# Kernel tuning notes

Measured on AMD Instinct MI355X. Metric: run time of the kernel, lower is better.

## Reference

```python
import jax, jax.numpy as jnp
import numpy as np

EPS = 1e-7
POS_THR = 0.7
NEG_THR = 0.3


def _make_boxes(key, shape):
    # corner-format boxes (x1, y1, x2, y2) in [0, 1]
    k1, k2 = jax.random.split(key)
    center = jax.random.uniform(k1, shape[:-1] + (2,), minval=0.2, maxval=0.8)
    size = jax.random.uniform(k2, shape[:-1] + (2,), minval=0.05, maxval=0.3)
    return jnp.concatenate([center - size / 2, center + size / 2], axis=-1)


def setup_inputs() -> dict:
    key = jax.random.key(0)
    B, M, N, C = 16, 128, 25200, 80
    k1, k2, k3, k4, k5, k6 = jax.random.split(key, 6)
    label_box = _make_boxes(k1, (B, M, 4))
    # zero-pad ~half the label slots (padding convention detected via != 0)
    valid = jax.random.uniform(k2, (B, M)) < 0.5
    label_box = label_box * valid[:, :, None].astype(jnp.float32)
    label_cls = jax.random.randint(k3, (B, M), 0, C)
    # predictions: jittered copies of label boxes so positive matches exist
    assign = jnp.arange(N) % M  # [N]
    box = label_box[:, assign, :] + 0.01 * jax.random.normal(k4, (B, N, 4))
    prb = jax.random.uniform(k5, (B, N), minval=0.01, maxval=0.99)
    cls_logits = jax.random.normal(k6, (B, N, C))
    cls = jax.nn.softmax(cls_logits, axis=-1)
    return {
        'label_box': label_box,
        'box': box,
        'prb': prb,
        'cls': cls,
        'label_cls': label_cls,
    }


def _iou_matrix(a, b):
    # a: [B, M, 4], b: [B, N, 4] corner boxes -> [B, M, N]
    a = a[:, :, None, :]
    b = b[:, None, :, :]
    ix1 = jnp.maximum(a[..., 0], b[..., 0])
    iy1 = jnp.maximum(a[..., 1], b[..., 1])
    ix2 = jnp.minimum(a[..., 2], b[..., 2])
    iy2 = jnp.minimum(a[..., 3], b[..., 3])
    inter = jnp.clip(ix2 - ix1, 0) * jnp.clip(iy2 - iy1, 0)
    area_a = jnp.clip(a[..., 2] - a[..., 0], 0) * jnp.clip(a[..., 3] - a[..., 1], 0)
    area_b = jnp.clip(b[..., 2] - b[..., 0], 0) * jnp.clip(b[..., 3] - b[..., 1], 0)
    union = area_a + area_b - inter
    return inter / (union + EPS)


def _ciou_loss(b1, b2):
    # elementwise CIoU loss between matched corner boxes [..., 4]
    ix1 = jnp.maximum(b1[..., 0], b2[..., 0])
    iy1 = jnp.maximum(b1[..., 1], b2[..., 1])
    ix2 = jnp.minimum(b1[..., 2], b2[..., 2])
    iy2 = jnp.minimum(b1[..., 3], b2[..., 3])
    inter = jnp.clip(ix2 - ix1, 0) * jnp.clip(iy2 - iy1, 0)
    w1 = jnp.clip(b1[..., 2] - b1[..., 0], 0)
    h1 = jnp.clip(b1[..., 3] - b1[..., 1], 0)
    w2 = jnp.clip(b2[..., 2] - b2[..., 0], 0)
    h2 = jnp.clip(b2[..., 3] - b2[..., 1], 0)
    union = w1 * h1 + w2 * h2 - inter
    iou = inter / (union + EPS)
    # enclosing box diagonal
    cw = jnp.maximum(b1[..., 2], b2[..., 2]) - jnp.minimum(b1[..., 0], b2[..., 0])
    ch = jnp.maximum(b1[..., 3], b2[..., 3]) - jnp.minimum(b1[..., 1], b2[..., 1])
    c2 = cw * cw + ch * ch + EPS
    # center distance
    dx = (b1[..., 0] + b1[..., 2] - b2[..., 0] - b2[..., 2]) / 2
    dy = (b1[..., 1] + b1[..., 3] - b2[..., 1] - b2[..., 3]) / 2
    rho2 = dx * dx + dy * dy
    v = (4.0 / (jnp.pi ** 2)) * jnp.square(
        jnp.arctan(w1 / (h1 + EPS)) - jnp.arctan(w2 / (h2 + EPS)))
    alpha = v / (1.0 - iou + v + EPS)
    ciou = iou - rho2 / c2 - alpha * v
    return 1.0 - ciou


def _masked_mean(x, m):
    m = m.astype(x.dtype)
    return jnp.sum(x * m) / jnp.maximum(jnp.sum(m), 1.0)


def reference(label_box, box, prb, cls, label_cls):
    # returns [box_loss, prb_loss, cls_loss]
    mask = jnp.any(label_box != 0, axis=-1)  # [B, M] valid GT slots
    iou_m = _iou_matrix(label_box, box)       # [B, M, N]
    iou_m = iou_m * mask[:, :, None].astype(iou_m.dtype)
    detect_idx = jnp.argmax(iou_m, axis=1)    # [B, N] best GT per prediction
    detect_iou = jnp.max(iou_m, axis=1)       # [B, N]
    detect_box = jnp.take_along_axis(label_box, detect_idx[:, :, None], axis=1)
    detect_cls = jnp.take_along_axis(label_cls, detect_idx, axis=1)
    pos = detect_iou > POS_THR
    neg = (detect_iou > 0.0) & (detect_iou < NEG_THR)

    box_loss = _masked_mean(_ciou_loss(detect_box, box), pos)

    p = jnp.clip(prb, EPS, 1.0 - EPS)
    prb_loss = _masked_mean(-jnp.log(p), pos) + _masked_mean(-jnp.log(1.0 - p), neg)

    pc = jnp.clip(cls, EPS, 1.0)
    nll = -jnp.log(jnp.take_along_axis(pc, detect_cls[:, :, None], axis=-1)[..., 0])
    cls_loss = _masked_mean(nll, pos)

    return jnp.stack([box_loss, prb_loss, cls_loss])
```

## Files before the change

### kernel.cpp

```cpp
#include <hip/hip_runtime.h>
#include <math.h>

#define EPSF 1e-7f

constexpr int B = 16, M = 128, N = 25200, C = 80;
constexpr int THREADS = 256;
constexpr int KN = 2;
constexpr int NPB = THREADS * KN;
constexpr int NBLK_X = (N + NPB - 1) / NPB;

__device__ __forceinline__ double wave_sum(double v) {
#pragma unroll
    for (int off = 32; off > 0; off >>= 1) v += __shfl_down(v, off, 64);
    return v;
}

__global__ __launch_bounds__(256) void detect_main(
    const float* __restrict__ label_box, const float* __restrict__ box,
    const float* __restrict__ prb, const float* __restrict__ cls,
    const int* __restrict__ label_cls, double* __restrict__ partial)
{
    __shared__ float4 s_lb[M];
    __shared__ float  s_area[M];
    __shared__ int    s_idx[M];
    __shared__ int    s_cls[M];
    __shared__ int    s_cnt[4];
    __shared__ int    s_mcount;

    const int b = blockIdx.y;
    const int t = threadIdx.x;
    const int lane = t & 63;
    const int wid  = t >> 6;

    float4 a4 = make_float4(0.f, 0.f, 0.f, 0.f);
    bool valid = false;
    if (t < M) {
        a4 = reinterpret_cast<const float4*>(label_box)[b * M + t];
        valid = (a4.x != 0.f) | (a4.y != 0.f) | (a4.z != 0.f) | (a4.w != 0.f);
        s_cls[t] = label_cls[b * M + t];
    }
    unsigned long long ball = __ballot(valid);
    if (lane == 0) s_cnt[wid] = __popcll(ball);
    __syncthreads();
    if (valid) {
        int base = 0;
#pragma unroll
        for (int w = 0; w < 4; ++w) if (w < wid) base += s_cnt[w];
        int c = base + __popcll(ball & ((1ull << lane) - 1ull));
        s_lb[c]   = a4;
        s_area[c] = fmaxf(a4.z - a4.x, 0.0f) * fmaxf(a4.w - a4.y, 0.0f);
        s_idx[c]  = t;
    }
    if (t == 0) s_mcount = s_cnt[0] + s_cnt[1] + s_cnt[2] + s_cnt[3];
    __syncthreads();
    const int mc = s_mcount;

    const int nbase = blockIdx.x * NPB + t;
    float4 bx[KN];
    float  areab[KN];
    bool   act[KN];
    float  ibest[KN], ubest[KN];
    int    bc[KN];
#pragma unroll
    for (int k = 0; k < KN; ++k) {
        const int n = nbase + k * THREADS;
        act[k] = (n < N);
        bx[k] = act[k] ? reinterpret_cast<const float4*>(box)[b * N + n]
                       : make_float4(0.f, 0.f, 0.f, 0.f);
        float w2 = fmaxf(bx[k].z - bx[k].x, 0.0f);
        float h2 = fmaxf(bx[k].w - bx[k].y, 0.0f);
        areab[k] = w2 * h2;
        ibest[k] = 0.0f;
        ubest[k] = 1.0f;
        bc[k]    = 0;
    }

    for (int m = 0; m < mc; ++m) {
        const float4 a  = s_lb[m];
        const float  aa = s_area[m];
#pragma unroll
        for (int k = 0; k < KN; ++k) {
            float ix1 = fmaxf(a.x, bx[k].x);
            float iy1 = fmaxf(a.y, bx[k].y);
            float ix2 = fminf(a.z, bx[k].z);
            float iy2 = fminf(a.w, bx[k].w);
            float inter = fmaxf(ix2 - ix1, 0.0f) * fmaxf(iy2 - iy1, 0.0f);
            float uni_e = ((aa + areab[k]) - inter) + EPSF;
            if (inter * ubest[k] > ibest[k] * uni_e) {
                ibest[k] = inter; ubest[k] = uni_e; bc[k] = m;
            }
        }
    }

    double v_pos = 0.0, v_neg = 0.0, v_ciou = 0.0;
    double v_logp = 0.0, v_log1mp = 0.0, v_nll = 0.0;

#pragma unroll
    for (int k = 0; k < KN; ++k) {
        if (!act[k]) continue;
        const int n = nbase + k * THREADS;
        const float best = ibest[k] / ubest[k];
        const bool pos = best > 0.7f;
        const bool neg = (best > 0.0f) && (best < 0.3f);
        if (!(pos | neg)) continue;

        const float p = fminf(fmaxf(prb[b * N + n], EPSF), 1.0f - EPSF);

        if (pos) {
            v_pos += 1.0;
            v_logp += (double)(-logf(p));

            float4 a = s_lb[bc[k]];
            float ix1 = fmaxf(a.x, bx[k].x);
            float iy1 = fmaxf(a.y, bx[k].y);
            float ix2 = fminf(a.z, bx[k].z);
            float iy2 = fminf(a.w, bx[k].w);
            float inter = fmaxf(ix2 - ix1, 0.0f) * fmaxf(iy2 - iy1, 0.0f);
            float w1 = fmaxf(a.z - a.x, 0.0f);
            float h1 = fmaxf(a.w - a.y, 0.0f);
            float w2 = fmaxf(bx[k].z - bx[k].x, 0.0f);
            float h2 = fmaxf(bx[k].w - bx[k].y, 0.0f);
            float uni = w1 * h1 + w2 * h2 - inter;
            float iou = inter / (uni + EPSF);
            float cw = fmaxf(a.z, bx[k].z) - fminf(a.x, bx[k].x);
            float ch = fmaxf(a.w, bx[k].w) - fminf(a.y, bx[k].y);
            float c2 = cw * cw + ch * ch + EPSF;
            float dx = (a.x + a.z - bx[k].x - bx[k].z) * 0.5f;
            float dy = (a.y + a.w - bx[k].y - bx[k].w) * 0.5f;
            float rho2 = dx * dx + dy * dy;
            float dat = atanf(w1 / (h1 + EPSF)) - atanf(w2 / (h2 + EPSF));
            float v = 0.40528473456935109f * dat * dat;
            float alpha = v / (1.0f - iou + v + EPSF);
            float ciou = iou - rho2 / c2 - alpha * v;
            v_ciou += (double)(1.0f - ciou);

            int dcls = s_cls[s_idx[bc[k]]];
            float pc = cls[(size_t)(b * N + n) * C + dcls];
            pc = fminf(fmaxf(pc, EPSF), 1.0f);
            v_nll += (double)(-logf(pc));
        } else {
            v_neg += 1.0;
            v_log1mp += (double)(-logf(1.0f - p));
        }
    }

    __shared__ double s_red[6][4];
    double vals[6] = { v_pos, v_neg, v_ciou, v_logp, v_log1mp, v_nll };
#pragma unroll
    for (int kk = 0; kk < 6; ++kk) {
        double v = wave_sum(vals[kk]);
        if (lane == 0) s_red[kk][wid] = v;
    }
    __syncthreads();

    if (t == 0) {
        const int bid = blockIdx.y * gridDim.x + blockIdx.x;
#pragma unroll
        for (int kk = 0; kk < 6; ++kk)
            partial[(size_t)bid * 6 + kk] =
                s_red[kk][0] + s_red[kk][1] + s_red[kk][2] + s_red[kk][3];
    }
}

__global__ __launch_bounds__(256) void detect_finalize(
    const double* __restrict__ partial, int nblocks, float* __restrict__ out)
{
    double acc[6] = {0.0, 0.0, 0.0, 0.0, 0.0, 0.0};
    for (int i = threadIdx.x; i < nblocks; i += 256) {
#pragma unroll
        for (int k = 0; k < 6; ++k) acc[k] += partial[(size_t)i * 6 + k];
    }

    __shared__ double s_red[6][4];
    const int lane = threadIdx.x & 63;
    const int wid  = threadIdx.x >> 6;
#pragma unroll
    for (int k = 0; k < 6; ++k) {
        double v = wave_sum(acc[k]);
        if (lane == 0) s_red[k][wid] = v;
    }
    __syncthreads();

    if (threadIdx.x == 0) {
        double tot[6];
#pragma unroll
        for (int k = 0; k < 6; ++k)
            tot[k] = s_red[k][0] + s_red[k][1] + s_red[k][2] + s_red[k][3];

        const double npos = fmax(tot[0], 1.0);
        const double nneg = fmax(tot[1], 1.0);
        out[0] = (float)(tot[2] / npos);
        out[1] = (float)(tot[3] / npos + tot[4] / nneg);
        out[2] = (float)(tot[5] / npos);
    }
}

extern "C" void kernel_launch(void* const* d_in, const int* in_sizes, int n_in,
                              void* d_out, int out_size, void* d_ws, size_t ws_size,
                              hipStream_t stream) {
    const float* label_box = (const float*)d_in[0];
    const float* box       = (const float*)d_in[1];
    const float* prb       = (const float*)d_in[2];
    const float* cls       = (const float*)d_in[3];
    const int*   label_cls = (const int*)d_in[4];
    float*  out     = (float*)d_out;
    double* partial = (double*)d_ws;

    dim3 grid(NBLK_X, B);
    detect_main<<<grid, THREADS, 0, stream>>>(label_box, box, prb, cls, label_cls, partial);
    detect_finalize<<<1, 256, 0, stream>>>(partial, NBLK_X * B, out);
}
```

Before: 31.83 us.

## Use 48 blocks per batch with exact partition and a tail wave

The grid is reshaped from 50 blocks of 512 predictions to 48 blocks of 525 predictions per image, which gives 768 blocks. Each thread handles two predictions, and one rotating wave per block handles the 13 leftover ones. The argmax comparison now uses the sum of areas instead of the union, which is monotone-equivalent for the ratio comparison and saves a subtract per pair. The IoU is recomputed once in the epilogue. The class lookup is precompacted so the epilogue needs one fewer shared-memory indirection. The intent is to cut tail blocks and inner-loop ALU work, at the cost of an unbalanced extra pass by one wave per block.

```diff
diff --git a/kernel.cpp b/kernel.cpp
--- a/kernel.cpp
+++ b/kernel.cpp
@@ -5,14 +5,30 @@
 
 constexpr int B = 16, M = 128, N = 25200, C = 80;
 constexpr int THREADS = 256;
-constexpr int KN = 2;
-constexpr int NPB = THREADS * KN;
-constexpr int NBLK_X = (N + NPB - 1) / NPB;
+constexpr int NBLK_X = 48;
+constexpr int NPB = N / NBLK_X;
+constexpr int NBLOCKS = NBLK_X * B;
 
 __device__ __forceinline__ double wave_sum(double v) {
 #pragma unroll
     for (int off = 32; off > 0; off >>= 1) v += __shfl_down(v, off, 64);
     return v;
+}
+
+__device__ __forceinline__ void argmax_one(
+    const float4* s_lb, const float* s_area, int mc, const float4& bx,
+    float areabe, float& ibest, float& Sbest, int& bc)
+{
+    for (int m = 0; m < mc; ++m) {
+        const float4 a = s_lb[m];
+        float ix1 = fmaxf(a.x, bx.x);
+        float iy1 = fmaxf(a.y, bx.y);
+        float ix2 = fminf(a.z, bx.z);
+        float iy2 = fminf(a.w, bx.w);
+        float inter = fmaxf(ix2 - ix1, 0.0f) * fmaxf(iy2 - iy1, 0.0f);
+        float S = s_area[m] + areabe;
+        if (inter * Sbest > ibest * S) { ibest = inter; Sbest = S; bc = m; }
+    }
 }
 
 __global__ __launch_bounds__(256) void detect_main(
@@ -22,8 +38,7 @@
 {
     __shared__ float4 s_lb[M];
     __shared__ float  s_area[M];
-    __shared__ int    s_idx[M];
-    __shared__ int    s_cls[M];
+    __shared__ int    s_ccls[M];
     __shared__ int    s_cnt[4];
     __shared__ int    s_mcount;
 
@@ -37,7 +52,6 @@
     if (t < M) {
         a4 = reinterpret_cast<const float4*>(label_box)[b * M + t];
         valid = (a4.x != 0.f) | (a4.y != 0.f) | (a4.z != 0.f) | (a4.w != 0.f);
-        s_cls[t] = label_cls[b * M + t];
     }
     unsigned long long ball = __ballot(valid);
     if (lane == 0) s_cnt[wid] = __popcll(ball);
@@ -49,60 +63,77 @@
         int c = base + __popcll(ball & ((1ull << lane) - 1ull));
         s_lb[c]   = a4;
         s_area[c] = fmaxf(a4.z - a4.x, 0.0f) * fmaxf(a4.w - a4.y, 0.0f);
-        s_idx[c]  = t;
+        s_ccls[c] = label_cls[b * M + t];
     }
     if (t == 0) s_mcount = s_cnt[0] + s_cnt[1] + s_cnt[2] + s_cnt[3];
     __syncthreads();
     const int mc = s_mcount;
 
-    const int nbase = blockIdx.x * NPB + t;
-    float4 bx[KN];
-    float  areab[KN];
-    bool   act[KN];
-    float  ibest[KN], ubest[KN];
-    int    bc[KN];
-#pragma unroll
-    for (int k = 0; k < KN; ++k) {
-        const int n = nbase + k * THREADS;
-        act[k] = (n < N);
-        bx[k] = act[k] ? reinterpret_cast<const float4*>(box)[b * N + n]
-                       : make_float4(0.f, 0.f, 0.f, 0.f);
-        float w2 = fmaxf(bx[k].z - bx[k].x, 0.0f);
-        float h2 = fmaxf(bx[k].w - bx[k].y, 0.0f);
-        areab[k] = w2 * h2;
-        ibest[k] = 0.0f;
-        ubest[k] = 1.0f;
-        bc[k]    = 0;
-    }
-
+    const int nbase = blockIdx.x * NPB;
+    const int n0 = nbase + t;
+    const int n1 = nbase + 256 + t;
+
+    float4 bx0 = reinterpret_cast<const float4*>(box)[b * N + n0];
+    float4 bx1 = reinterpret_cast<const float4*>(box)[b * N + n1];
+    float areab0 = fmaxf(bx0.z - bx0.x, 0.0f) * fmaxf(bx0.w - bx0.y, 0.0f);
+    float areab1 = fmaxf(bx1.z - bx1.x, 0.0f) * fmaxf(bx1.w - bx1.y, 0.0f);
+    float areabe0 = areab0 + EPSF;
+    float areabe1 = areab1 + EPSF;
+    float ibest0 = 0.0f, Sbest0 = 1.0f; int bc0 = 0;
+    float ibest1 = 0.0f, Sbest1 = 1.0f; int bc1 = 0;
+
+#pragma unroll 2
     for (int m = 0; m < mc; ++m) {
         const float4 a  = s_lb[m];
         const float  aa = s_area[m];
-#pragma unroll
-        for (int k = 0; k < KN; ++k) {
-            float ix1 = fmaxf(a.x, bx[k].x);
-            float iy1 = fmaxf(a.y, bx[k].y);
-            float ix2 = fminf(a.z, bx[k].z);
-            float iy2 = fminf(a.w, bx[k].w);
+        {
+            float ix1 = fmaxf(a.x, bx0.x);
+            float iy1 = fmaxf(a.y, bx0.y);
+            float ix2 = fminf(a.z, bx0.z);
+            float iy2 = fminf(a.w, bx0.w);
             float inter = fmaxf(ix2 - ix1, 0.0f) * fmaxf(iy2 - iy1, 0.0f);
-            float uni_e = ((aa + areab[k]) - inter) + EPSF;
-            if (inter * ubest[k] > ibest[k] * uni_e) {
-                ibest[k] = inter; ubest[k] = uni_e; bc[k] = m;
-            }
+            float S = aa + areabe0;
+            if (inter * Sbest0 > ibest0 * S) { ibest0 = inter; Sbest0 = S; bc0 = m; }
         }
+        {
+            float ix1 = fmaxf(a.x, bx1.x);
+            float iy1 = fmaxf(a.y, bx1.y);
+            float ix2 = fminf(a.z, bx1.z);
+            float iy2 = fminf(a.w, bx1.w);
+            float inter = fmaxf(ix2 - ix1, 0.0f) * fmaxf(iy2 - iy1, 0.0f);
+            float S = aa + areabe1;
+            if (inter * Sbest1 > ibest1 * S) { ibest1 = inter; Sbest1 = S; bc1 = m; }
+        }
+    }
+
+    const int tw = blockIdx.x & 3;
+    const bool tact = (wid == tw) && (lane < (NPB - 512));
+    const int n2 = nbase + 512 + lane;
+    float4 bx2 = make_float4(0.f, 0.f, 0.f, 0.f);
+    float areab2 = 0.0f, areabe2 = EPSF;
+    float ibest2 = 0.0f, Sbest2 = 1.0f; int bc2 = 0;
+    if (tact) {
+        bx2 = reinterpret_cast<const float4*>(box)[b * N + n2];
+        areab2 = fmaxf(bx2.z - bx2.x, 0.0f) * fmaxf(bx2.w - bx2.y, 0.0f);
+        areabe2 = areab2 + EPSF;
+        argmax_one(s_lb, s_area, mc, bx2, areabe2, ibest2, Sbest2, bc2);
     }
 
     double v_pos = 0.0, v_neg = 0.0, v_ciou = 0.0;
     double v_logp = 0.0, v_log1mp = 0.0, v_nll = 0.0;
 
-#pragma unroll
-    for (int k = 0; k < KN; ++k) {
-        if (!act[k]) continue;
-        const int n = nbase + k * THREADS;
-        const float best = ibest[k] / ubest[k];
+    auto epilogue = [&](int n, const float4& bx, float areab, int bc) {
+        const float4 a = s_lb[bc];
+        float ix1 = fmaxf(a.x, bx.x);
+        float iy1 = fmaxf(a.y, bx.y);
+        float ix2 = fminf(a.z, bx.z);
+        float iy2 = fminf(a.w, bx.w);
+        float inter = fmaxf(ix2 - ix1, 0.0f) * fmaxf(iy2 - iy1, 0.0f);
+        float best = inter / (((s_area[bc] + areab) - inter) + EPSF);
+
         const bool pos = best > 0.7f;
         const bool neg = (best > 0.0f) && (best < 0.3f);
-        if (!(pos | neg)) continue;
+        if (!(pos | neg)) return;
 
         const float p = fminf(fmaxf(prb[b * N + n], EPSF), 1.0f - EPSF);
 
@@ -110,23 +141,17 @@
             v_pos += 1.0;
             v_logp += (double)(-logf(p));
 
-            float4 a = s_lb[bc[k]];
-            float ix1 = fmaxf(a.x, bx[k].x);
-            float iy1 = fmaxf(a.y, bx[k].y);
-            float ix2 = fminf(a.z, bx[k].z);
-            float iy2 = fminf(a.w, bx[k].w);
-            float inter = fmaxf(ix2 - ix1, 0.0f) * fmaxf(iy2 - iy1, 0.0f);
             float w1 = fmaxf(a.z - a.x, 0.0f);
             float h1 = fmaxf(a.w - a.y, 0.0f);
-            float w2 = fmaxf(bx[k].z - bx[k].x, 0.0f);
-            float h2 = fmaxf(bx[k].w - bx[k].y, 0.0f);
+            float w2 = fmaxf(bx.z - bx.x, 0.0f);
+            float h2 = fmaxf(bx.w - bx.y, 0.0f);
             float uni = w1 * h1 + w2 * h2 - inter;
             float iou = inter / (uni + EPSF);
-            float cw = fmaxf(a.z, bx[k].z) - fminf(a.x, bx[k].x);
-            float ch = fmaxf(a.w, bx[k].w) - fminf(a.y, bx[k].y);
+            float cw = fmaxf(a.z, bx.z) - fminf(a.x, bx.x);
+            float ch = fmaxf(a.w, bx.w) - fminf(a.y, bx.y);
             float c2 = cw * cw + ch * ch + EPSF;
-            float dx = (a.x + a.z - bx[k].x - bx[k].z) * 0.5f;
-            float dy = (a.y + a.w - bx[k].y - bx[k].w) * 0.5f;
+            float dx = (a.x + a.z - bx.x - bx.z) * 0.5f;
+            float dy = (a.y + a.w - bx.y - bx.w) * 0.5f;
             float rho2 = dx * dx + dy * dy;
             float dat = atanf(w1 / (h1 + EPSF)) - atanf(w2 / (h2 + EPSF));
             float v = 0.40528473456935109f * dat * dat;
@@ -134,14 +159,19 @@
             float ciou = iou - rho2 / c2 - alpha * v;
             v_ciou += (double)(1.0f - ciou);
 
-            int dcls = s_cls[s_idx[bc[k]]];
-            float pc = cls[(size_t)(b * N + n) * C + dcls];
+            float pc = cls[(size_t)(b * N + n) * C + s_ccls[bc]];
             pc = fminf(fmaxf(pc, EPSF), 1.0f);
             v_nll += (double)(-logf(pc));
         } else {
             v_neg += 1.0;
             v_log1mp += (double)(-logf(1.0f - p));
         }
+    };
+
+    if (mc > 0) {
+        epilogue(n0, bx0, areab0, bc0);
+        epilogue(n1, bx1, areab1, bc1);
+        if (tact) epilogue(n2, bx2, areab2, bc2);
     }
 
     __shared__ double s_red[6][4];
@@ -163,10 +193,10 @@
 }
 
 __global__ __launch_bounds__(256) void detect_finalize(
-    const double* __restrict__ partial, int nblocks, float* __restrict__ out)
+    const double* __restrict__ partial, float* __restrict__ out)
 {
     double acc[6] = {0.0, 0.0, 0.0, 0.0, 0.0, 0.0};
-    for (int i = threadIdx.x; i < nblocks; i += 256) {
+    for (int i = threadIdx.x; i < NBLOCKS; i += 256) {
 #pragma unroll
         for (int k = 0; k < 6; ++k) acc[k] += partial[(size_t)i * 6 + k];
     }
@@ -208,5 +238,5 @@
 
     dim3 grid(NBLK_X, B);
     detect_main<<<grid, THREADS, 0, stream>>>(label_box, box, prb, cls, label_cls, partial);
-    detect_finalize<<<1, 256, 0, stream>>>(partial, NBLK_X * B, out);
-}
+    detect_finalize<<<1, 256, 0, stream>>>(partial, out);
+}
```

Result: slower. 33.17 us (+4.2%).
